# Performance work log

Measured on AMD Instinct MI355X. Metric: run time of the kernel, lower is better.

The kernel has to match this reference:

```python
import jax, jax.numpy as jnp
import numpy as np

BETA = 0.25  # commitment loss weight (beta)
EPS_NORM = 1e-12  # F.normalize eps


def l2norm(t):
    return t / jnp.clip(jnp.linalg.norm(t, axis=-1, keepdims=True), EPS_NORM)


def setup_inputs() -> dict:
    key = jax.random.key(0)
    k1, k2 = jax.random.split(key)
    z = jax.random.normal(k1, (16, 256, 32, 32), dtype=jnp.float32)
    # EmbeddingEMA with kmeans_init=False: weight = l2norm(randn(n_embed, dim))
    weight = l2norm(jax.random.normal(k2, (8192, 256), dtype=jnp.float32))
    return {"z": z, "weight": weight}


def reference(z, weight):
    # z: [B, C, H, W] -> [B, H, W, C], l2-normalized per token
    zc = l2norm(jnp.transpose(z, (0, 2, 3, 1)))
    B, H, W, D = zc.shape
    zf = zc.reshape(-1, D)  # [N, D]
    zf_d = jax.lax.stop_gradient(zf)
    # negative squared L2 distance: -|z|^2 - |w|^2 + 2 z.w  -> argmax = nearest code
    d = (-jnp.sum(zf_d ** 2, axis=1, keepdims=True)
         - jnp.sum(weight ** 2, axis=1)
         + 2.0 * jnp.einsum('nd,kd->nk', zf_d, weight))  # [N, K]
    idx = jnp.argmax(d, axis=1)  # [N]
    z_q = weight[idx].reshape(B, H, W, D)  # codebook gather
    # commitment loss: beta * mean((sg(z_q) - z)^2)
    loss = BETA * jnp.mean((jax.lax.stop_gradient(z_q) - zc) ** 2)
    # straight-through estimator
    z_q = zc + jax.lax.stop_gradient(z_q - zc)
    z_q = jnp.transpose(z_q, (0, 3, 1, 2))  # back to [B, C, H, W]
    return z_q, loss, idx
```

## Files before the change

### kernel.cpp

```cpp
#include <hip/hip_runtime.h>
#include <math.h>

#define BB   16
#define CC   256
#define HW   1024
#define NN   16384
#define DD   256
#define KK   8192
#define ZQ_SIZE 4194304
#define MARGIN 0.017f
#define GCAP 8192
#define RSPLIT 8

typedef __attribute__((ext_vector_type(8))) short short8;
typedef __attribute__((ext_vector_type(4))) float f32x4;

static __device__ inline unsigned short f2bf(float x) {
    unsigned int u = __float_as_uint(x);
    unsigned int r = (u + 0x7fff + ((u >> 16) & 1)) >> 16;
    return (unsigned short)r;
}

static __device__ inline unsigned long long pack_key(float s, int k) {
    unsigned int bits = __float_as_uint(s);
    unsigned int o = (bits & 0x80000000u) ? ~bits : (bits | 0x80000000u);
    return ((unsigned long long)o << 32) | (unsigned int)(~k);
}

__global__ __launch_bounds__(256) void wsqwb_kernel(const float* __restrict__ W,
                                                    float* __restrict__ wsq,
                                                    unsigned short* __restrict__ wb,
                                                    int* __restrict__ gcnt,
                                                    int* __restrict__ oflow) {
    if (blockIdx.x == 0) {
        gcnt[threadIdx.x] = 0;
        if (threadIdx.x == 0) *oflow = 0;
    }
    {
        const int lane = threadIdx.x & 63;
        const int k = blockIdx.x * 4 + (threadIdx.x >> 6);
        float4 v = *(const float4*)(W + (size_t)k * DD + lane * 4);
        float s = v.x * v.x + v.y * v.y + v.z * v.z + v.w * v.w;
        #pragma unroll
        for (int off = 32; off; off >>= 1) s += __shfl_down(s, off);
        if (lane == 0) wsq[k] = s;
    }
    if (blockIdx.x < 1024) {
        const int ch = blockIdx.x * 256 + threadIdx.x;
        const int c = (ch >> 7) & 7;
        const int r = ch & 127;
        const int kt = ch >> 12, dc = (ch >> 10) & 3;
        const int k = kt * 128 + r;
        const int d0 = dc * 64 + c * 8;
        const float4 v0 = *(const float4*)(W + (size_t)k * DD + d0);
        const float4 v1 = *(const float4*)(W + (size_t)k * DD + d0 + 4);
        uint4 out;
        out.x = (unsigned int)f2bf(v0.x) | ((unsigned int)f2bf(v0.y) << 16);
        out.y = (unsigned int)f2bf(v0.z) | ((unsigned int)f2bf(v0.w) << 16);
        out.z = (unsigned int)f2bf(v1.x) | ((unsigned int)f2bf(v1.y) << 16);
        out.w = (unsigned int)f2bf(v1.z) | ((unsigned int)f2bf(v1.w) << 16);
        *(uint4*)(wb + (size_t)ch * 8) = out;
    }
}

__global__ __launch_bounds__(256) void normalize_kernel(const float* __restrict__ z,
                                                        float* __restrict__ zn,
                                                        float* __restrict__ znsq,
                                                        unsigned short* __restrict__ zb) {
    __shared__ float tile[64][257];
    __shared__ float s_nrm[64];
    const int t   = threadIdx.x;
    const int b   = blockIdx.x >> 4;
    const int hw0 = (blockIdx.x & 15) * 64;

    #pragma unroll
    for (int cg = 0; cg < 16; ++cg) {
        int c  = cg * 16 + (t >> 4);
        int hw = (t & 15) * 4;
        float4 v = *(const float4*)(z + ((size_t)(b * CC + c) << 10) + hw0 + hw);
        tile[hw + 0][c] = v.x;
        tile[hw + 1][c] = v.y;
        tile[hw + 2][c] = v.z;
        tile[hw + 3][c] = v.w;
    }
    __syncthreads();
    if (t < 64) {
        float s = 0.f;
        #pragma unroll 8
        for (int c = 0; c < 256; ++c) { float v = tile[t][c]; s += v * v; }
        float nrm = sqrtf(s);
        nrm = fmaxf(nrm, 1e-12f);
        s_nrm[t] = nrm;
        znsq[(size_t)b * HW + hw0 + t] = s / (nrm * nrm);
    }
    __syncthreads();
    const int n0 = b * HW + hw0;
    for (int r = 0; r < 64; ++r) {
        zn[(size_t)(n0 + r) * DD + t] = tile[r][t] / s_nrm[r];
    }
    const int r    = t & 63;
    const int mt   = n0 >> 7;
    const int rg   = (n0 & 127) + r;
    const float nrm = s_nrm[r];
    #pragma unroll
    for (int loop = 0; loop < 8; ++loop) {
        int comb = loop * 4 + (t >> 6);
        int dc = comb >> 3, c = comb & 7;
        int d0 = dc * 64 + c * 8;
        uint4 out;
        out.x = (unsigned int)f2bf(tile[r][d0 + 0] / nrm) | ((unsigned int)f2bf(tile[r][d0 + 1] / nrm) << 16);
        out.y = (unsigned int)f2bf(tile[r][d0 + 2] / nrm) | ((unsigned int)f2bf(tile[r][d0 + 3] / nrm) << 16);
        out.z = (unsigned int)f2bf(tile[r][d0 + 4] / nrm) | ((unsigned int)f2bf(tile[r][d0 + 5] / nrm) << 16);
        out.w = (unsigned int)f2bf(tile[r][d0 + 6] / nrm) | ((unsigned int)f2bf(tile[r][d0 + 7] / nrm) << 16);
        *(uint4*)(zb + (size_t)(mt * 4 + dc) * 8192 + (size_t)(c * 128 + rg) * 8) = out;
    }
}

__global__ __launch_bounds__(512, 2) void score_kernel(const unsigned short* __restrict__ zb,
                                                       const unsigned short* __restrict__ wb,
                                                       const float* __restrict__ wsqv,
                                                       float* __restrict__ cmax) {
    __shared__ __align__(16) unsigned short sT[2][16384];
    __shared__ __align__(16) unsigned short sC[2][16384];
    __shared__ float rowbuf[8][260];
    __shared__ __align__(16) float swsq[256];

    const int tid  = threadIdx.x;
    const int w    = tid >> 6;
    const int lane = tid & 63;
    const int wr   = w >> 2;
    const int wc   = w & 3;
    const int q    = lane >> 4, c15 = lane & 15;
    const int kt   = blockIdx.x & 31;
    const int mt   = blockIdx.x >> 5;
    const int mtb  = mt * 8;
    const int ktb  = kt * 8;

    if (tid < 256) swsq[tid] = wsqv[kt * 256 + tid];

    const int sh = (w >> 1) & 1;
    auto stage = [&](int bf, int dc) {
        const unsigned short* gs = (w < 4)
            ? (zb + (size_t)(mtb + sh * 4 + dc) * 8192)
            : (wb + (size_t)(ktb + sh * 4 + dc) * 8192);
        unsigned short* ld = (w < 4) ? &sT[bf][sh * 8192] : &sC[bf][sh * 8192];
        #pragma unroll
        for (int i = 0; i < 8; ++i) {
            const int eo = ((w & 1) * 8 + i) << 9;
            __builtin_amdgcn_global_load_lds(
                (const __attribute__((address_space(1))) void*)(gs + eo + lane * 8),
                (__attribute__((address_space(3))) void*)(ld + eo), 16, 0, 0);
        }
    };

    f32x4 acc[8][4];
    #pragma unroll
    for (int fi = 0; fi < 8; ++fi)
        #pragma unroll
        for (int fj = 0; fj < 4; ++fj)
            acc[fi][fj] = (f32x4){0.f, 0.f, 0.f, 0.f};

    const int tHalf = wc >> 1;
    const int tRow0 = (wc & 1) * 64 + c15;

    stage(0, 0);
    stage(1, 1);
    asm volatile("s_waitcnt vmcnt(8)" ::: "memory");
    __builtin_amdgcn_s_barrier();

    #pragma unroll
    for (int t = 0; t < 4; ++t) {
        const int bf = t & 1;
        const unsigned short* sTb = &sT[bf][tHalf * 8192];
        const unsigned short* sCb = &sC[bf][wr * 8192];
        #pragma unroll
        for (int ks = 0; ks < 2; ++ks) {
            const int ca = (ks * 4 + q) * 128;
            short8 tfr[4];
            #pragma unroll
            for (int fj = 0; fj < 4; ++fj)
                tfr[fj] = *(const short8*)(sTb + (size_t)(ca + tRow0 + fj * 16) * 8);
            #pragma unroll
            for (int fih = 0; fih < 2; ++fih) {
                short8 cfr[4];
                #pragma unroll
                for (int f = 0; f < 4; ++f)
                    cfr[f] = *(const short8*)(sCb + (size_t)(ca + fih * 64 + f * 16 + c15) * 8);
                __builtin_amdgcn_s_barrier();
                __builtin_amdgcn_s_setprio(1);
                #pragma unroll
                for (int f = 0; f < 4; ++f)
                    #pragma unroll
                    for (int fj = 0; fj < 4; ++fj)
                        acc[fih * 4 + f][fj] = __builtin_amdgcn_mfma_f32_16x16x32_bf16(
                            cfr[f], tfr[fj], acc[fih * 4 + f][fj], 0, 0, 0);
                __builtin_amdgcn_s_setprio(0);
                __builtin_amdgcn_s_barrier();
            }
        }
        asm volatile("s_waitcnt lgkmcnt(0)" ::: "memory");
        __builtin_amdgcn_s_barrier();
        if (t == 0)      { stage(0, 2); asm volatile("s_waitcnt vmcnt(8)" ::: "memory"); }
        else if (t == 1) { stage(1, 3); asm volatile("s_waitcnt vmcnt(8)" ::: "memory"); }
        else if (t == 2) {              asm volatile("s_waitcnt vmcnt(0)" ::: "memory"); }
        __builtin_amdgcn_s_barrier();
    }

    f32x4 wq4[8];
    #pragma unroll
    for (int fi = 0; fi < 8; ++fi)
        wq4[fi] = *(const f32x4*)(&swsq[wr * 128 + fi * 16 + q * 4]);

    #pragma unroll
    for (int fj = 0; fj < 4; ++fj) {
        float vg[4];
        #pragma unroll
        for (int gl = 0; gl < 4; ++gl) {
            float v = -INFINITY;
            #pragma unroll
            for (int f2 = 0; f2 < 2; ++f2) {
                const int fi = gl * 2 + f2;
                #pragma unroll
                for (int rg = 0; rg < 4; ++rg)
                    v = fmaxf(v, 2.0f * acc[fi][fj][rg] - wq4[fi][rg]);
            }
            v = fmaxf(v, __shfl_xor(v, 16));
            v = fmaxf(v, __shfl_xor(v, 32));
            vg[gl] = v;
        }
        const float val = (q == 0) ? vg[0] : (q == 1) ? vg[1] : (q == 2) ? vg[2] : vg[3];
        rowbuf[wr * 4 + q][wc * 64 + fj * 16 + c15] = val;
    }
    __syncthreads();
    {
        const int row = tid >> 1, half = tid & 1;
        float4 o;
        o.x = rowbuf[half * 4 + 0][row];
        o.y = rowbuf[half * 4 + 1][row];
        o.z = rowbuf[half * 4 + 2][row];
        o.w = rowbuf[half * 4 + 3][row];
        *(float4*)(cmax + (size_t)(mt * 256 + row) * 256 + kt * 8 + half * 4) = o;
    }
}

__global__ __launch_bounds__(256) void cand_kernel(const float* __restrict__ cmax,
                                                   unsigned int* __restrict__ gseg,
                                                   int* __restrict__ gcnt,
                                                   unsigned long long* __restrict__ packed,
                                                   int* __restrict__ nflag,
                                                   int* __restrict__ oflow) {
    const int t = threadIdx.x, wv = t >> 6, lane = t & 63;
    const int n = blockIdx.x * 4 + wv;
    float4 c4 = *(const float4*)(cmax + (size_t)n * 256 + lane * 4);
    float lm = fmaxf(fmaxf(c4.x, c4.y), fmaxf(c4.z, c4.w));
    #pragma unroll
    for (int off = 1; off <= 32; off <<= 1) lm = fmaxf(lm, __shfl_xor(lm, off));
    const float thresh = lm - MARGIN;
    if (lane == 0) { packed[n] = 0ull; nflag[n] = 0; }
    float g4[4] = {c4.x, c4.y, c4.z, c4.w};
    #pragma unroll
    for (int j = 0; j < 4; ++j) {
        int g = lane * 4 + j;
        if (g4[j] >= thresh) {
            int pos = atomicAdd(&gcnt[g], 1);
            if (pos < GCAP) gseg[(size_t)g * GCAP + pos] = (unsigned int)n;
            else { nflag[n] = 1; atomicAdd(oflow, 1); }
        }
    }
}

__global__ __launch_bounds__(256) void rescore_kernel(const float* __restrict__ zn,
                                                      const float* __restrict__ W,
                                                      const float* __restrict__ wsqv,
                                                      const float* __restrict__ znsq,
                                                      const unsigned int* __restrict__ gseg,
                                                      const int* __restrict__ gcnt,
                                                      unsigned long long* __restrict__ packed) {
    __shared__ float sW[32 * 260];
    __shared__ float znr[4][2][256];

    const int t = threadIdx.x;
    const int g   = blockIdx.x >> 3;
    const int sub = blockIdx.x & 7;
    int cnt = gcnt[g]; if (cnt > GCAP) cnt = GCAP;
    if (cnt <= sub * 8) return;

    {
        int c = t >> 3, i = t & 7;
        const float4* src = (const float4*)(W + (size_t)g * 8192 + c * 256 + i * 32);
        #pragma unroll
        for (int j = 0; j < 8; ++j)
            *(float4*)(sW + c * 260 + i * 32 + j * 4) = src[j];
    }
    __syncthreads();

    const int wv = t >> 6, lane = t & 63;
    const int h = lane >> 5, c = lane & 31;
    const int k = g * 32 + c;
    const float wq = wsqv[k];
    const float4* wrow = (const float4*)(sW + c * 260);

    for (int base = (sub * 4 + wv) * 2; base < cnt; base += RSPLIT * 8) {
        int idx = base + h; if (idx >= cnt) idx = base;
        int n = (int)gseg[(size_t)g * GCAP + idx];
        *(float4*)(&znr[wv][h][c * 8])     = *(const float4*)(zn + (size_t)n * DD + c * 8);
        *(float4*)(&znr[wv][h][c * 8 + 4]) = *(const float4*)(zn + (size_t)n * DD + c * 8 + 4);
        float d = 0.f;
        #pragma unroll
        for (int j = 0; j < 64; ++j) {
            float4 wv4 = wrow[j];
            float4 zv  = *(const float4*)(&znr[wv][h][j * 4]);
            d += wv4.x * zv.x + wv4.y * zv.y + wv4.z * zv.z + wv4.w * zv.w;
        }
        float s = (-znsq[n] - wq) + 2.0f * d;
        unsigned long long key = pack_key(s, k);
        #pragma unroll
        for (int off = 1; off <= 16; off <<= 1) {
            unsigned long long ok = __shfl_xor(key, off);
            if (ok > key) key = ok;
        }
        if (c == 0) atomicMax(packed + n, key);
    }
}

__global__ __launch_bounds__(256) void fullscan_kernel(const float* __restrict__ zn,
                                                       const float* __restrict__ W,
                                                       const float* __restrict__ wsqv,
                                                       const float* __restrict__ znsq,
                                                       const int* __restrict__ nflag,
                                                       const int* __restrict__ oflow,
                                                       unsigned long long* __restrict__ packed) {
    if (*oflow == 0) return;
    const int t = threadIdx.x, wv = t >> 6, lane = t & 63;
    const int code = lane >> 1, part = lane & 1;
    for (int n = blockIdx.x * 4 + wv; n < NN; n += gridDim.x * 4) {
        if (!nflag[n]) continue;
        float zsq = znsq[n];
        unsigned long long best = 0ull;
        for (int gg = 0; gg < 256; ++gg) {
            int k = gg * 32 + code;
            const float4* wrp = (const float4*)(W + (size_t)k * DD + part * 128);
            const float4* zrp = (const float4*)(zn + (size_t)n * DD + part * 128);
            float d = 0.f;
            #pragma unroll
            for (int jj = 0; jj < 32; ++jj) {
                float4 a = zrp[jj], b = wrp[jj];
                d += a.x * b.x + a.y * b.y + a.z * b.z + a.w * b.w;
            }
            d += __shfl_xor(d, 1);
            unsigned long long key = pack_key((-zsq - wsqv[k]) + 2.0f * d, k);
            if (key > best) best = key;
        }
        #pragma unroll
        for (int off = 1; off <= 32; off <<= 1) {
            unsigned long long ok = __shfl_xor(best, off);
            if (ok > best) best = ok;
        }
        if (lane == 0) atomicMax(packed + n, best);
    }
}

__global__ __launch_bounds__(256) void gatherfin_kernel(const float* __restrict__ W,
                                                        const unsigned long long* __restrict__ packed,
                                                        float* __restrict__ idxf,
                                                        float* __restrict__ partials,
                                                        float* __restrict__ zq) {
    __shared__ int sbk[64];
    const int t   = threadIdx.x;
    const int b   = blockIdx.x >> 4;
    const int hw0 = (blockIdx.x & 15) * 64;
    if (t < 64) {
        int n = b * HW + hw0 + t;
        unsigned long long key = packed[n];
        int k = (int)((~(unsigned int)key) & 0x3FFFu);
        unsigned int o = (unsigned int)(key >> 32);
        unsigned int bits = (o & 0x80000000u) ? (o & 0x7FFFFFFFu) : ~o;
        float s = __uint_as_float(bits);
        sbk[t] = k;
        idxf[n] = (float)k;
        float cc = -s;
        #pragma unroll
        for (int off = 32; off; off >>= 1) cc += __shfl_down(cc, off);
        if (t == 0) partials[blockIdx.x] = cc;
    }
    __syncthreads();
    const int hw  = t & 63;
    const int c0  = (t >> 6) * 4;
    const int row = sbk[hw];
    #pragma unroll
    for (int cg = 0; cg < 16; ++cg) {
        int c = cg * 16 + c0;
        float4 v = *(const float4*)(W + (size_t)row * DD + c);
        size_t base = ((size_t)(b * CC + c) << 10) + hw0 + hw;
        zq[base]        = v.x;
        zq[base + 1024] = v.y;
        zq[base + 2048] = v.z;
        zq[base + 3072] = v.w;
    }
}

__global__ __launch_bounds__(256) void loss_final_kernel(const float* __restrict__ partials,
                                                         float* __restrict__ out_loss) {
    __shared__ float wsum[4];
    const int t = threadIdx.x;
    float v = partials[t];
    #pragma unroll
    for (int off = 32; off; off >>= 1) v += __shfl_down(v, off);
    if ((t & 63) == 0) wsum[t >> 6] = v;
    __syncthreads();
    if (t == 0) {
        float tot = wsum[0] + wsum[1] + wsum[2] + wsum[3];
        *out_loss = 0.25f * (tot / (float)ZQ_SIZE);
    }
}

extern "C" void kernel_launch(void* const* d_in, const int* in_sizes, int n_in,
                              void* d_out, int out_size, void* d_ws, size_t ws_size,
                              hipStream_t stream) {
    const float* z = (const float*)d_in[0];
    const float* W = (const float*)d_in[1];

    float* out   = (float*)d_out;
    float* zq    = out;
    float* loss  = out + ZQ_SIZE;
    float* idxf  = out + ZQ_SIZE + 1;

    float* ws       = (float*)d_ws;
    float* zn       = ws;
    float* znsq     = zn + (size_t)NN * DD;
    float* wsqv     = znsq + NN;
    float* partials = wsqv + KK;
    int*   gcnt     = (int*)(partials + 256);
    int*   oflow    = gcnt + 256;
    int*   nflag    = oflow + 64;
    unsigned short* zb = (unsigned short*)(nflag + NN);
    unsigned short* wb = zb + (size_t)NN * DD;
    float* cmax     = (float*)(wb + (size_t)KK * DD);
    unsigned int* gseg = (unsigned int*)(cmax + (size_t)NN * 256);
    unsigned long long* packed = (unsigned long long*)(gseg + (size_t)256 * GCAP);

    wsqwb_kernel     <<<KK / 4, 256, 0, stream>>>(W, wsqv, wb, gcnt, oflow);
    normalize_kernel <<<BB * 16, 256, 0, stream>>>(z, zn, znsq, zb);
    score_kernel     <<<(NN / 256) * (KK / 256), 512, 0, stream>>>(zb, wb, wsqv, cmax);
    cand_kernel      <<<NN / 4, 256, 0, stream>>>(cmax, gseg, gcnt, packed, nflag, oflow);
    rescore_kernel   <<<256 * RSPLIT, 256, 0, stream>>>(zn, W, wsqv, znsq, gseg, gcnt, packed);
    fullscan_kernel  <<<64, 256, 0, stream>>>(zn, W, wsqv, znsq, nflag, oflow, packed);
    gatherfin_kernel <<<BB * 16, 256, 0, stream>>>(W, packed, idxf, partials, zq);
    loss_final_kernel<<<1, 256, 0, stream>>>(partials, loss);
}
```

Measured before the change: 238.3 us.

## Interleave codebook tile prefetch with MFMA phases in distance GEMM

Restructures the main bf16 distance GEMM loop into four phases per K-chunk. Each phase loads a quarter of the codebook fragments and issues a slice of the next tile's global-to-LDS copies, instead of issuing one bulk stage after the chunk's compute. All token fragments for the chunk are loaded once up front. The aim is to hide global-load latency behind MFMA work and shorten the exposed waits between chunks. In exchange the loop has more barriers and sched_barrier fences, holds more fragment registers live, and waits on vmcnt(0) at each chunk boundary.

```diff
diff --git a/kernel.cpp b/kernel.cpp
--- a/kernel.cpp
+++ b/kernel.cpp
@@ -139,13 +139,13 @@
     if (tid < 256) swsq[tid] = wsqv[kt * 256 + tid];
 
     const int sh = (w >> 1) & 1;
-    auto stage = [&](int bf, int dc) {
+    auto stage2 = [&](int bf, int dc, int i0) {
         const unsigned short* gs = (w < 4)
             ? (zb + (size_t)(mtb + sh * 4 + dc) * 8192)
             : (wb + (size_t)(ktb + sh * 4 + dc) * 8192);
         unsigned short* ld = (w < 4) ? &sT[bf][sh * 8192] : &sC[bf][sh * 8192];
         #pragma unroll
-        for (int i = 0; i < 8; ++i) {
+        for (int i = i0; i < i0 + 2; ++i) {
             const int eo = ((w & 1) * 8 + i) << 9;
             __builtin_amdgcn_global_load_lds(
                 (const __attribute__((address_space(1))) void*)(gs + eo + lane * 8),
@@ -163,8 +163,8 @@
     const int tHalf = wc >> 1;
     const int tRow0 = (wc & 1) * 64 + c15;
 
-    stage(0, 0);
-    stage(1, 1);
+    stage2(0, 0, 0); stage2(0, 0, 2); stage2(0, 0, 4); stage2(0, 0, 6);
+    stage2(1, 1, 0); stage2(1, 1, 2); stage2(1, 1, 4); stage2(1, 1, 6);
     asm volatile("s_waitcnt vmcnt(8)" ::: "memory");
     __builtin_amdgcn_s_barrier();
 
@@ -173,37 +173,45 @@
         const int bf = t & 1;
         const unsigned short* sTb = &sT[bf][tHalf * 8192];
         const unsigned short* sCb = &sC[bf][wr * 8192];
-        #pragma unroll
-        for (int ks = 0; ks < 2; ++ks) {
-            const int ca = (ks * 4 + q) * 128;
-            short8 tfr[4];
-            #pragma unroll
-            for (int fj = 0; fj < 4; ++fj)
-                tfr[fj] = *(const short8*)(sTb + (size_t)(ca + tRow0 + fj * 16) * 8);
-            #pragma unroll
-            for (int fih = 0; fih < 2; ++fih) {
-                short8 cfr[4];
+        short8 tfr[2][4];
+        #pragma unroll
+        for (int p = 0; p < 4; ++p) {
+            if (p == 0) {
                 #pragma unroll
-                for (int f = 0; f < 4; ++f)
-                    cfr[f] = *(const short8*)(sCb + (size_t)(ca + fih * 64 + f * 16 + c15) * 8);
-                __builtin_amdgcn_s_barrier();
-                __builtin_amdgcn_s_setprio(1);
-                #pragma unroll
-                for (int f = 0; f < 4; ++f)
+                for (int ks = 0; ks < 2; ++ks)
                     #pragma unroll
                     for (int fj = 0; fj < 4; ++fj)
-                        acc[fih * 4 + f][fj] = __builtin_amdgcn_mfma_f32_16x16x32_bf16(
-                            cfr[f], tfr[fj], acc[fih * 4 + f][fj], 0, 0, 0);
-                __builtin_amdgcn_s_setprio(0);
-                __builtin_amdgcn_s_barrier();
+                        tfr[ks][fj] = *(const short8*)(sTb +
+                            (size_t)((ks * 4 + q) * 128 + tRow0 + fj * 16) * 8);
             }
-        }
-        asm volatile("s_waitcnt lgkmcnt(0)" ::: "memory");
-        __builtin_amdgcn_s_barrier();
-        if (t == 0)      { stage(0, 2); asm volatile("s_waitcnt vmcnt(8)" ::: "memory"); }
-        else if (t == 1) { stage(1, 3); asm volatile("s_waitcnt vmcnt(8)" ::: "memory"); }
-        else if (t == 2) {              asm volatile("s_waitcnt vmcnt(0)" ::: "memory"); }
-        __builtin_amdgcn_s_barrier();
+            short8 cfr[2][2];
+            #pragma unroll
+            for (int ks = 0; ks < 2; ++ks)
+                #pragma unroll
+                for (int f = 0; f < 2; ++f)
+                    cfr[ks][f] = *(const short8*)(sCb +
+                        (size_t)((ks * 4 + q) * 128 + p * 32 + f * 16 + c15) * 8);
+            if (t == 1)      stage2(0, 2, p * 2);
+            else if (t == 2) stage2(1, 3, p * 2);
+            __builtin_amdgcn_s_barrier();
+            asm volatile("s_waitcnt lgkmcnt(0)" ::: "memory");
+            __builtin_amdgcn_sched_barrier(0);
+            __builtin_amdgcn_s_setprio(1);
+            #pragma unroll
+            for (int ks = 0; ks < 2; ++ks)
+                #pragma unroll
+                for (int f = 0; f < 2; ++f)
+                    #pragma unroll
+                    for (int fj = 0; fj < 4; ++fj)
+                        acc[p * 2 + f][fj] = __builtin_amdgcn_mfma_f32_16x16x32_bf16(
+                            cfr[ks][f], tfr[ks][fj], acc[p * 2 + f][fj], 0, 0, 0);
+            __builtin_amdgcn_s_setprio(0);
+            __builtin_amdgcn_s_barrier();
+        }
+        if (t < 3) {
+            asm volatile("s_waitcnt vmcnt(0)" ::: "memory");
+            __builtin_amdgcn_s_barrier();
+        }
     }
 
     f32x4 wq4[8];
```

New measurement: 233.2 us. 2.1% less time.
